# Optimization experiments

Hardware: AMD Instinct MI355X
Metric: run time of the kernel (lower is better)

## Reference

```python
import jax, jax.numpy as jnp
import numpy as np

N_NODES = 100000
N_EDGES = 3200000
D_IN = 256
D_OUT = 256


def setup_inputs() -> dict:
    key = jax.random.key(0)
    k1, k2, k3, k4, k5, k6 = jax.random.split(key, 6)
    x = jax.random.normal(k1, (N_NODES, D_IN), dtype=jnp.float32)
    edge_src = jax.random.randint(k2, (N_EDGES,), 0, N_NODES, dtype=jnp.int32)
    edge_dst = jax.random.randint(k3, (N_EDGES,), 0, N_NODES, dtype=jnp.int32)
    edge_weight = jax.random.uniform(k4, (N_EDGES,), dtype=jnp.float32)
    weight = jax.random.normal(k5, (D_IN, D_OUT), dtype=jnp.float32) * 0.02
    bias = jax.random.uniform(k6, (D_OUT,), dtype=jnp.float32)
    return {"x": x, "edge_src": edge_src, "edge_dst": edge_dst,
            "edge_weight": edge_weight, "weight": weight, "bias": bias}


def reference(x, edge_src, edge_dst, edge_weight, weight, bias):
    # support = X @ W  (dense GEMM)
    support = x @ weight  # [N, D_OUT]
    # output = A @ support, A given as COO edges (dst <- src with weight)
    msgs = support[edge_src] * edge_weight[:, None]  # [E, D_OUT]
    out = jax.ops.segment_sum(msgs, edge_dst, num_segments=N_NODES)  # [N, D_OUT]
    return out + bias
```

## Files before the change

kernel.cpp:

```cpp
#include <hip/hip_runtime.h>
#include <hip/hip_bf16.h>

#define N_NODES 100000
#define N_EDGES 3200000
#define DDIM    256
#define M_PAD   100096
#define NBKT    782
#define BCAP    4608
#define EPB_A   4096

typedef __attribute__((ext_vector_type(8))) short short8;
typedef __attribute__((ext_vector_type(4))) float f32x4;

typedef const __attribute__((address_space(1))) void gvoid_t;
typedef __attribute__((address_space(3))) void lvoid_t;

__device__ __forceinline__ void load_lds16(const void* g, void* l) {
  __builtin_amdgcn_global_load_lds((gvoid_t*)g, (lvoid_t*)l, 16, 0, 0);
}

__device__ __forceinline__ unsigned short f2bf(float f) {
  __hip_bfloat16 h = __float2bfloat16(f);
  return *(unsigned short*)&h;
}
__device__ __forceinline__ float bflo(unsigned u) { return __uint_as_float(u << 16); }
__device__ __forceinline__ float bfhi(unsigned u) { return __uint_as_float(u & 0xffff0000u); }

__global__ void conv_x_kernel(const float* __restrict__ x, unsigned short* __restrict__ xb) {
  size_t i = (size_t)blockIdx.x * blockDim.x + threadIdx.x;
  size_t idx = i * 4;
  if (idx >= (size_t)N_NODES * DDIM) return;
  float4 v = *(const float4*)(x + idx);
  ushort4 o;
  o.x = f2bf(v.x); o.y = f2bf(v.y); o.z = f2bf(v.z); o.w = f2bf(v.w);
  *(ushort4*)(xb + idx) = o;
}

__global__ void conv_w_kernel(const float* __restrict__ w, unsigned short* __restrict__ wt) {
  int t = blockIdx.x * blockDim.x + threadIdx.x;
  int n = t >> 8, k = t & 255;
  wt[t] = f2bf(w[k * 256 + n]);
}

__global__ __launch_bounds__(256) void gemm_kernel(const unsigned short* __restrict__ xb,
                                                   const unsigned short* __restrict__ wt,
                                                   unsigned short* __restrict__ sup) {
  __shared__ unsigned short As[128 * 32];
  __shared__ unsigned short Bs[128 * 32];
  const int tid  = threadIdx.x;
  const int w    = tid >> 6;
  const int lane = tid & 63;
  const int quad = lane >> 4;
  const int l15  = lane & 15;
  const int wr   = w >> 1, wc = w & 1;
  const int m0 = blockIdx.x * 128;
  const int n0 = blockIdx.y * 128;

  f32x4 acc[4][4] = {};

  const int srow   = lane >> 2;
  const int schunk = (lane & 3) * 8;

  for (int kt = 0; kt < 256; kt += 32) {
#pragma unroll
    for (int i = 0; i < 2; ++i) {
      int r = w * 32 + i * 16 + srow;
      load_lds16(xb + ((size_t)(m0 + r) * 256 + kt + schunk),
                 As + (w * 32 + i * 16) * 32);
      load_lds16(wt + ((size_t)(n0 + r) * 256 + kt + schunk),
                 Bs + (w * 32 + i * 16) * 32);
    }
    __syncthreads();

    short8 a[4], b[4];
#pragma unroll
    for (int mi = 0; mi < 4; ++mi)
      a[mi] = *(const short8*)(As + (wr * 64 + mi * 16 + l15) * 32 + quad * 8);
#pragma unroll
    for (int ni = 0; ni < 4; ++ni)
      b[ni] = *(const short8*)(Bs + (wc * 64 + ni * 16 + l15) * 32 + quad * 8);

#pragma unroll
    for (int mi = 0; mi < 4; ++mi)
#pragma unroll
      for (int ni = 0; ni < 4; ++ni)
        acc[mi][ni] = __builtin_amdgcn_mfma_f32_16x16x32_bf16(a[mi], b[ni], acc[mi][ni], 0, 0, 0);
    __syncthreads();
  }

#pragma unroll
  for (int mi = 0; mi < 4; ++mi) {
#pragma unroll
    for (int r = 0; r < 4; ++r) {
      size_t row = (size_t)(m0 + wr * 64 + mi * 16 + quad * 4 + r);
#pragma unroll
      for (int ni = 0; ni < 4; ++ni) {
        int col = n0 + wc * 64 + ni * 16 + l15;
        sup[row * 256 + col] = f2bf(acc[mi][ni][r]);
      }
    }
  }
}

__global__ __launch_bounds__(256) void binA_kernel(const int* __restrict__ src,
                                                   const int* __restrict__ dst,
                                                   const float* __restrict__ wgt,
                                                   int* __restrict__ gcur,
                                                   unsigned long long* __restrict__ region) {
  __shared__ unsigned long long staged[EPB_A];
  __shared__ unsigned short sbkt[EPB_A];
  __shared__ int lhist[NBKT];
  __shared__ int lstart[NBKT];
  __shared__ int lcur[NBKT];
  __shared__ int gb[NBKT];
  __shared__ int csum[256];

  const int t = threadIdx.x;
  const int e0 = blockIdx.x * EPB_A;
  const int ecnt = min(EPB_A, N_EDGES - e0);

  for (int i = t; i < NBKT; i += 256) lhist[i] = 0;
  __syncthreads();
  for (int k = t; k < ecnt; k += 256)
    atomicAdd(&lhist[dst[e0 + k] >> 7], 1);
  __syncthreads();

  int i0 = 4 * t;
  int a0 = (i0 + 0 < NBKT) ? lhist[i0 + 0] : 0;
  int a1 = (i0 + 1 < NBKT) ? lhist[i0 + 1] : 0;
  int a2 = (i0 + 2 < NBKT) ? lhist[i0 + 2] : 0;
  int a3 = (i0 + 3 < NBKT) ? lhist[i0 + 3] : 0;
  int s = a0 + a1 + a2 + a3;
  csum[t] = s;
  __syncthreads();
  for (int off = 1; off < 256; off <<= 1) {
    int v = (t >= off) ? csum[t - off] : 0;
    __syncthreads();
    csum[t] += v;
    __syncthreads();
  }
  int base = csum[t] - s;
  if (i0 + 0 < NBKT) lstart[i0 + 0] = base; base += a0;
  if (i0 + 1 < NBKT) lstart[i0 + 1] = base; base += a1;
  if (i0 + 2 < NBKT) lstart[i0 + 2] = base; base += a2;
  if (i0 + 3 < NBKT) lstart[i0 + 3] = base;
  __syncthreads();

  for (int i = t; i < NBKT; i += 256) {
    int c = lhist[i];
    int off = c ? atomicAdd(&gcur[i], c) : 0;
    gb[i] = i * BCAP + off;
    lcur[i] = lstart[i];
  }
  __syncthreads();

  for (int k = t; k < ecnt; k += 256) {
    int d  = dst[e0 + k];
    int sr = src[e0 + k];
    float w = wgt[e0 + k];
    int b = d >> 7;
    int p = atomicAdd(&lcur[b], 1);
    staged[p] = ((unsigned long long)__float_as_uint(w) << 32) |
                ((unsigned)(d & 127) << 17) | (unsigned)sr;
    sbkt[p] = (unsigned short)b;
  }
  __syncthreads();

  for (int j = t; j < ecnt; j += 256) {
    int b = sbkt[j];
    int addr = gb[b] + (j - lstart[b]);
    if (addr < (b + 1) * BCAP) region[addr] = staged[j];
  }
}

__global__ __launch_bounds__(256) void csrB_kernel(unsigned long long* __restrict__ region,
                                                   const int* __restrict__ gcur,
                                                   int2* __restrict__ rowse) {
  __shared__ unsigned long long lcsr[BCAP];
  __shared__ int lhist[128], loff[128], lcur[128];
  const int t = threadIdx.x;
  const int b = blockIdx.x;
  const int cnt = min(gcur[b], BCAP);
  const int base = b * BCAP;

  if (t < 128) lhist[t] = 0;
  __syncthreads();
  for (int j = t; j < cnt; j += 256) {
    unsigned lo = (unsigned)(region[base + j] & 0xffffffffu);
    atomicAdd(&lhist[(lo >> 17) & 127], 1);
  }
  __syncthreads();
  if (t < 128) loff[t] = lhist[t];
  __syncthreads();
  for (int off = 1; off < 128; off <<= 1) {
    int v = (t >= off && t < 128) ? loff[t - off] : 0;
    __syncthreads();
    if (t < 128) loff[t] += v;
    __syncthreads();
  }
  if (t < 128) { loff[t] -= lhist[t]; lcur[t] = loff[t]; }
  __syncthreads();
  for (int j = t; j < cnt; j += 256) {
    unsigned long long e = region[base + j];
    int dl = (int)((e >> 17) & 127);
    int p = atomicAdd(&lcur[dl], 1);
    lcsr[p] = e;
  }
  __syncthreads();
  for (int j = t; j < cnt; j += 256) region[base + j] = lcsr[j];
  if (t < 128) {
    int gd = b * 128 + t;
    if (gd < N_NODES) rowse[gd] = make_int2(base + loff[t], base + lcur[t]);
  }
}

__global__ __launch_bounds__(64) void gather_kernel(const unsigned long long* __restrict__ packed,
                                                    const int2* __restrict__ rowse,
                                                    const unsigned short* __restrict__ sup,
                                                    const float* __restrict__ bias,
                                                    float* __restrict__ out) {
  int n = blockIdx.x;
  int l = threadIdx.x;
  int c0 = l * 4;
  int2 se = rowse[n];
  int start = se.x, end = se.y;
  float4 bv = *(const float4*)(bias + c0);
  float a0 = bv.x, a1 = bv.y, a2 = bv.z, a3 = bv.w;

  int i = start;
  for (; i + 2 <= end; i += 2) {
    unsigned long long m0 = packed[i];
    unsigned long long m1 = packed[i + 1];
    int   s0 = (int)(m0 & 0x1ffffu);
    float w0 = __uint_as_float((unsigned)(m0 >> 32));
    int   s1 = (int)(m1 & 0x1ffffu);
    float w1 = __uint_as_float((unsigned)(m1 >> 32));
    uint2 p0 = *(const uint2*)(sup + (size_t)s0 * 256 + c0);
    uint2 p1 = *(const uint2*)(sup + (size_t)s1 * 256 + c0);
    a0 = fmaf(w0, bflo(p0.x), a0);
    a1 = fmaf(w0, bfhi(p0.x), a1);
    a2 = fmaf(w0, bflo(p0.y), a2);
    a3 = fmaf(w0, bfhi(p0.y), a3);
    a0 = fmaf(w1, bflo(p1.x), a0);
    a1 = fmaf(w1, bfhi(p1.x), a1);
    a2 = fmaf(w1, bflo(p1.y), a2);
    a3 = fmaf(w1, bfhi(p1.y), a3);
  }
  if (i < end) {
    unsigned long long m0 = packed[i];
    int   s0 = (int)(m0 & 0x1ffffu);
    float w0 = __uint_as_float((unsigned)(m0 >> 32));
    uint2 p0 = *(const uint2*)(sup + (size_t)s0 * 256 + c0);
    a0 = fmaf(w0, bflo(p0.x), a0);
    a1 = fmaf(w0, bfhi(p0.x), a1);
    a2 = fmaf(w0, bflo(p0.y), a2);
    a3 = fmaf(w0, bfhi(p0.y), a3);
  }
  *(float4*)(out + (size_t)n * 256 + c0) = make_float4(a0, a1, a2, a3);
}

extern "C" void kernel_launch(void* const* d_in, const int* in_sizes, int n_in,
                              void* d_out, int out_size, void* d_ws, size_t ws_size,
                              hipStream_t stream) {
  const float* x        = (const float*)d_in[0];
  const int*   edge_src = (const int*)d_in[1];
  const int*   edge_dst = (const int*)d_in[2];
  const float* edge_w   = (const float*)d_in[3];
  const float* weight   = (const float*)d_in[4];
  const float* bias     = (const float*)d_in[5];
  float* out = (float*)d_out;

  char* ws = (char*)d_ws;
  size_t off = 0;
  auto alloc = [&](size_t bytes) -> void* {
    void* p = ws + off;
    off = (off + bytes + 255) & ~(size_t)255;
    return p;
  };

  unsigned short* xb  = (unsigned short*)alloc((size_t)M_PAD * 256 * 2);
  unsigned short* wt  = (unsigned short*)alloc(256 * 256 * 2);
  unsigned short* sup = (unsigned short*)alloc((size_t)M_PAD * 256 * 2);

  char* xbb = (char*)xb;
  unsigned long long* region = (unsigned long long*)xbb;
  int*  gcur  = (int*)(xbb + (29u << 20));
  int2* rowse = (int2*)(xbb + (30u << 20));

  conv_x_kernel<<<25000, 256, 0, stream>>>(x, xb);
  conv_w_kernel<<<256, 256, 0, stream>>>(weight, wt);
  gemm_kernel<<<dim3(782, 2), 256, 0, stream>>>(xb, wt, sup);
  hipMemsetAsync(gcur, 0, NBKT * 4, stream);
  binA_kernel<<<(N_EDGES + EPB_A - 1) / EPB_A, 256, 0, stream>>>(edge_src, edge_dst, edge_w,
                                                                 gcur, region);
  csrB_kernel<<<NBKT, 256, 0, stream>>>(region, gcur, rowse);
  gather_kernel<<<N_NODES, 64, 0, stream>>>(region, rowse, sup, bias, out);
}
```

Before: 533.0 us.

## Sort edges by source range and gather multiple rows per wave in lockstep passes

The CSR build now sorts each destination row's edges into 16 sub-buckets keyed on the source index's high bits. The gather kernel is restructured so each wave handles 13 destination rows and sweeps the source ranges in 16 passes, so all concurrently running waves touch the same slice of the support matrix at once. This aims to improve L2/MALL hit rates on the random gathers from the bf16 support matrix. It costs more registers (13x4 accumulators), a serial while loop with data-dependent breaks, and less parallelism from fewer, larger blocks.

```diff
diff --git a/kernel.cpp b/kernel.cpp
--- a/kernel.cpp
+++ b/kernel.cpp
@@ -8,6 +8,8 @@
 #define NBKT    782
 #define BCAP    4608
 #define EPB_A   4096
+#define NPW     13
+#define GBLK    2048
 
 typedef __attribute__((ext_vector_type(8))) short short8;
 typedef __attribute__((ext_vector_type(4))) float f32x4;
@@ -177,86 +179,103 @@
                                                    const int* __restrict__ gcur,
                                                    int2* __restrict__ rowse) {
   __shared__ unsigned long long lcsr[BCAP];
-  __shared__ int lhist[128], loff[128], lcur[128];
+  __shared__ int lhist[2048];
+  __shared__ int csum[256];
   const int t = threadIdx.x;
   const int b = blockIdx.x;
   const int cnt = min(gcur[b], BCAP);
   const int base = b * BCAP;
 
-  if (t < 128) lhist[t] = 0;
+  for (int i = t; i < 2048; i += 256) lhist[i] = 0;
   __syncthreads();
   for (int j = t; j < cnt; j += 256) {
-    unsigned lo = (unsigned)(region[base + j] & 0xffffffffu);
-    atomicAdd(&lhist[(lo >> 17) & 127], 1);
-  }
-  __syncthreads();
-  if (t < 128) loff[t] = lhist[t];
-  __syncthreads();
-  for (int off = 1; off < 128; off <<= 1) {
-    int v = (t >= off && t < 128) ? loff[t - off] : 0;
-    __syncthreads();
-    if (t < 128) loff[t] += v;
-    __syncthreads();
-  }
-  if (t < 128) { loff[t] -= lhist[t]; lcur[t] = loff[t]; }
+    unsigned lo = (unsigned)region[base + j];
+    int key = (int)((((lo >> 17) & 127) << 4) | ((lo >> 13) & 15));
+    atomicAdd(&lhist[key], 1);
+  }
+  __syncthreads();
+  int loc[8], s = 0;
+#pragma unroll
+  for (int j = 0; j < 8; ++j) { loc[j] = lhist[8 * t + j]; s += loc[j]; }
+  csum[t] = s;
+  __syncthreads();
+  for (int off = 1; off < 256; off <<= 1) {
+    int v = (t >= off) ? csum[t - off] : 0;
+    __syncthreads();
+    csum[t] += v;
+    __syncthreads();
+  }
+  int run = csum[t] - s;
+#pragma unroll
+  for (int j = 0; j < 8; ++j) { lhist[8 * t + j] = run; run += loc[j]; }
+  __syncthreads();
+  if (t < 128) {
+    int gd = b * 128 + t;
+    if (gd < N_NODES) {
+      int st = lhist[t * 16];
+      int en = (t == 127) ? cnt : lhist[(t + 1) * 16];
+      rowse[gd] = make_int2(base + st, base + en);
+    }
+  }
   __syncthreads();
   for (int j = t; j < cnt; j += 256) {
     unsigned long long e = region[base + j];
-    int dl = (int)((e >> 17) & 127);
-    int p = atomicAdd(&lcur[dl], 1);
+    unsigned lo = (unsigned)e;
+    int key = (int)((((lo >> 17) & 127) << 4) | ((lo >> 13) & 15));
+    int p = atomicAdd(&lhist[key], 1);
     lcsr[p] = e;
   }
   __syncthreads();
   for (int j = t; j < cnt; j += 256) region[base + j] = lcsr[j];
-  if (t < 128) {
-    int gd = b * 128 + t;
-    if (gd < N_NODES) rowse[gd] = make_int2(base + loff[t], base + lcur[t]);
-  }
-}
-
-__global__ __launch_bounds__(64) void gather_kernel(const unsigned long long* __restrict__ packed,
-                                                    const int2* __restrict__ rowse,
-                                                    const unsigned short* __restrict__ sup,
-                                                    const float* __restrict__ bias,
-                                                    float* __restrict__ out) {
-  int n = blockIdx.x;
-  int l = threadIdx.x;
-  int c0 = l * 4;
-  int2 se = rowse[n];
-  int start = se.x, end = se.y;
+}
+
+__global__ __launch_bounds__(256) void gather_kernel(const unsigned long long* __restrict__ packed,
+                                                     const int2* __restrict__ rowse,
+                                                     const unsigned short* __restrict__ sup,
+                                                     const float* __restrict__ bias,
+                                                     float* __restrict__ out) {
+  const int wid  = blockIdx.x * 4 + (threadIdx.x >> 6);
+  const int lane = threadIdx.x & 63;
+  const int c0   = lane * 4;
+  const int n0   = wid * NPW;
   float4 bv = *(const float4*)(bias + c0);
-  float a0 = bv.x, a1 = bv.y, a2 = bv.z, a3 = bv.w;
-
-  int i = start;
-  for (; i + 2 <= end; i += 2) {
-    unsigned long long m0 = packed[i];
-    unsigned long long m1 = packed[i + 1];
-    int   s0 = (int)(m0 & 0x1ffffu);
-    float w0 = __uint_as_float((unsigned)(m0 >> 32));
-    int   s1 = (int)(m1 & 0x1ffffu);
-    float w1 = __uint_as_float((unsigned)(m1 >> 32));
-    uint2 p0 = *(const uint2*)(sup + (size_t)s0 * 256 + c0);
-    uint2 p1 = *(const uint2*)(sup + (size_t)s1 * 256 + c0);
-    a0 = fmaf(w0, bflo(p0.x), a0);
-    a1 = fmaf(w0, bfhi(p0.x), a1);
-    a2 = fmaf(w0, bflo(p0.y), a2);
-    a3 = fmaf(w0, bfhi(p0.y), a3);
-    a0 = fmaf(w1, bflo(p1.x), a0);
-    a1 = fmaf(w1, bfhi(p1.x), a1);
-    a2 = fmaf(w1, bflo(p1.y), a2);
-    a3 = fmaf(w1, bfhi(p1.y), a3);
-  }
-  if (i < end) {
-    unsigned long long m0 = packed[i];
-    int   s0 = (int)(m0 & 0x1ffffu);
-    float w0 = __uint_as_float((unsigned)(m0 >> 32));
-    uint2 p0 = *(const uint2*)(sup + (size_t)s0 * 256 + c0);
-    a0 = fmaf(w0, bflo(p0.x), a0);
-    a1 = fmaf(w0, bfhi(p0.x), a1);
-    a2 = fmaf(w0, bflo(p0.y), a2);
-    a3 = fmaf(w0, bfhi(p0.y), a3);
-  }
-  *(float4*)(out + (size_t)n * 256 + c0) = make_float4(a0, a1, a2, a3);
+
+  float a[NPW][4];
+  int cur[NPW], en[NPW];
+#pragma unroll
+  for (int p = 0; p < NPW; ++p) {
+    int n = n0 + p;
+    if (n < N_NODES) { int2 se = rowse[n]; cur[p] = se.x; en[p] = se.y; }
+    else             { cur[p] = 0; en[p] = 0; }
+    a[p][0] = bv.x; a[p][1] = bv.y; a[p][2] = bv.z; a[p][3] = bv.w;
+  }
+
+  for (int r = 0; r < 16; ++r) {
+#pragma unroll
+    for (int p = 0; p < NPW; ++p) {
+      int c = cur[p], e = en[p];
+      while (c < e) {
+        unsigned long long m = packed[c];
+        int src = (int)(m & 0x1ffffu);
+        if ((src >> 13) != r) break;
+        float w = __uint_as_float((unsigned)(m >> 32));
+        uint2 px = *(const uint2*)(sup + (size_t)src * 256 + c0);
+        a[p][0] = fmaf(w, bflo(px.x), a[p][0]);
+        a[p][1] = fmaf(w, bfhi(px.x), a[p][1]);
+        a[p][2] = fmaf(w, bflo(px.y), a[p][2]);
+        a[p][3] = fmaf(w, bfhi(px.y), a[p][3]);
+        ++c;
+      }
+      cur[p] = c;
+    }
+  }
+
+#pragma unroll
+  for (int p = 0; p < NPW; ++p) {
+    int n = n0 + p;
+    if (n < N_NODES)
+      *(float4*)(out + (size_t)n * 256 + c0) = make_float4(a[p][0], a[p][1], a[p][2], a[p][3]);
+  }
 }
 
 extern "C" void kernel_launch(void* const* d_in, const int* in_sizes, int n_in,
@@ -294,5 +313,5 @@
   binA_kernel<<<(N_EDGES + EPB_A - 1) / EPB_A, 256, 0, stream>>>(edge_src, edge_dst, edge_w,
                                                                  gcur, region);
   csrB_kernel<<<NBKT, 256, 0, stream>>>(region, gcur, rowse);
-  gather_kernel<<<N_NODES, 64, 0, stream>>>(region, rowse, sup, bias, out);
-}
+  gather_kernel<<<GBLK, 256, 0, stream>>>(region, rowse, sup, bias, out);
+}
```

Result: slower. 997.0 us (+87.1%).
